# Kernel optimization log

Hardware: AMD Instinct MI355X
Metric: run time of the kernel (lower is better)

## Reference

```python
import jax, jax.numpy as jnp
import numpy as np

IN_DIM, HID, MID, FFN, OUT = 384, 128, 1024, 512, 1024
B, T = 8, 4096
LN_EPS = 1e-5


def _legs_hippo(n: int) -> np.ndarray:
    # A[i, j] = P_i(2j/n - 1) * sqrt(2i + 1), Legendre via 3-term recurrence
    x = 2.0 * np.arange(n) / n - 1.0          # eval points, shape [n]
    P = np.zeros((n, n), dtype=np.float64)     # P[i] = P_i(x)
    P[0] = 1.0
    if n > 1:
        P[1] = x
    for i in range(1, n - 1):
        P[i + 1] = ((2 * i + 1) * x * P[i] - i * P[i - 1]) / (i + 1)
    A = P * np.sqrt(2.0 * np.arange(n) + 1.0)[:, None]
    # rescale so the 4096-step recurrence stays finite (A is a free Parameter,
    # so any test value is valid; unscaled LegS overflows fp32 in ~20 steps)
    s = np.linalg.norm(A, 2)
    return (A / (1.05 * s)).astype(np.float32)


def _layernorm(x, g, b):
    mu = jnp.mean(x, axis=-1, keepdims=True)
    var = jnp.var(x, axis=-1, keepdims=True)
    return (x - mu) * jax.lax.rsqrt(var + LN_EPS) * g + b


def setup_inputs() -> dict:
    key = jax.random.key(0)
    ks = jax.random.split(key, 16)

    def w(k, shape, fan_in):
        return jax.random.normal(k, shape, jnp.float32) * (1.0 / np.sqrt(fan_in))

    return {
        "padded_x": jax.random.normal(ks[0], (B, T, IN_DIM), jnp.float32),
        "seq_lens": jax.random.randint(ks[1], (B,), 1, T + 1, jnp.int32),
        "A": jnp.asarray(_legs_hippo(HID)),
        "enc_w1": w(ks[2], (IN_DIM, MID), IN_DIM), "enc_b1": jnp.zeros((MID,), jnp.float32),
        "enc_w2": w(ks[3], (MID, HID), MID), "enc_b2": jnp.zeros((HID,), jnp.float32),
        "proj_w": w(ks[4], (HID, MID), HID), "proj_b": jnp.zeros((MID,), jnp.float32),
        "ln1_g": jnp.ones((MID,), jnp.float32), "ln1_b": jnp.zeros((MID,), jnp.float32),
        "ffn_w1": w(ks[5], (MID, FFN), MID), "ffn_b1": jnp.zeros((FFN,), jnp.float32),
        "ffn_w2": w(ks[6], (FFN, OUT), FFN), "ffn_b2": jnp.zeros((OUT,), jnp.float32),
        "ln2_g": jnp.ones((OUT,), jnp.float32), "ln2_b": jnp.zeros((OUT,), jnp.float32),
        "out_w": w(ks[7], (OUT, OUT), OUT), "out_b": jnp.zeros((OUT,), jnp.float32),
    }


def reference(padded_x, seq_lens, A, enc_w1, enc_b1, enc_w2, enc_b2,
              proj_w, proj_b, ln1_g, ln1_b, ffn_w1, ffn_b1, ffn_w2, ffn_b2,
              ln2_g, ln2_b, out_w, out_b):
    # encoder: Linear -> GELU(exact) -> Linear   [B, T, HID]
    h_mid = jax.nn.gelu(padded_x @ enc_w1 + enc_b1, approximate=False)
    seqs_bx = h_mid @ enc_w2 + enc_b2

    # masked linear recurrence h_t = A @ h_{t-1} + Bx_t via lax.scan over time
    xs = jnp.swapaxes(seqs_bx, 0, 1)           # [T, B, HID]
    ts = jnp.arange(xs.shape[0])

    def step(h, inp):
        x_t, t = inp
        upd = h @ A.T + x_t                     # (A @ h)^T batched
        mask = (t < seq_lens)[:, None]          # [B, 1]
        return jnp.where(mask, upd, h), None

    h0 = jnp.zeros((padded_x.shape[0], A.shape[0]), padded_x.dtype)
    batch_h, _ = jax.lax.scan(step, h0, (xs, ts))

    # decoder
    projected = batch_h @ proj_w + proj_b
    norm_h = _layernorm(projected, ln1_g, ln1_b)
    ffn_out = jax.nn.gelu(norm_h @ ffn_w1 + ffn_b1, approximate=False) @ ffn_w2 + ffn_b2
    ffn_out = ffn_out + projected               # residual (requires OUT == MID)
    norm_ffn = _layernorm(ffn_out, ln2_g, ln2_b)
    return norm_ffn @ out_w + out_b             # [B, OUT]
```

## Files before the change

kernel.cpp:

```cpp
#include <hip/hip_runtime.h>

typedef __attribute__((ext_vector_type(8))) short short8;
typedef __attribute__((ext_vector_type(4))) short short4v;
typedef __attribute__((ext_vector_type(4))) float float4v;

__device__ __forceinline__ float bf2f(short s) {
  union { float f; unsigned u; } cv; cv.u = ((unsigned)(unsigned short)s) << 16; return cv.f;
}
__device__ __forceinline__ short f2bf(float f) {
  union { float f; unsigned u; } cv; cv.f = f;
  unsigned u = cv.u;
  unsigned r = u + 0x7FFFu + ((u >> 16) & 1u);
  return (short)(r >> 16);
}
__device__ __forceinline__ float gelu_f(float v) {
  return 0.5f * v * (1.0f + erff(v * 0.70710678118654752440f));
}
__device__ __forceinline__ void glds16(const short* g, short* l) {
  __builtin_amdgcn_global_load_lds(
      (const __attribute__((address_space(1))) void*)g,
      (__attribute__((address_space(3))) void*)l, 16, 0, 0);
}

__global__ __launch_bounds__(256) void enc_fused(
    const short* __restrict__ xB, const short* __restrict__ w1T,
    const short* __restrict__ w2T, const float* __restrict__ b1,
    float* __restrict__ encP, const int* __restrict__ seq_lens)
{
  int m0 = blockIdx.x * 64;
  { int b = m0 >> 12, t = m0 & 4095; if (t >= seq_lens[b]) return; }
  int nc0 = blockIdx.y * 2;

  __shared__ __align__(16) short As[64 * 64];
  __shared__ __align__(16) short Ws[128 * 64];
  __shared__ __align__(16) short midb[64 * 128];

  int tid = threadIdx.x, lane = tid & 63, wave = tid >> 6;
  int l15 = lane & 15, quad = lane >> 4;
  int lr = lane >> 3, lseg = lane & 7;

  float4v accO[4][2];
#pragma unroll
  for (int i = 0; i < 4; i++)
#pragma unroll
    for (int j = 0; j < 2; j++) accO[i][j] = 0;

  for (int nci = 0; nci < 2; ++nci) {
    int nc = nc0 + nci;
    float4v accM[4][2];
#pragma unroll
    for (int i = 0; i < 4; i++)
#pragma unroll
      for (int j = 0; j < 2; j++) accM[i][j] = 0;

    for (int ks = 0; ks < 6; ++ks) {
      int kk = ks * 64;
#pragma unroll
      for (int i = 0; i < 2; i++) {
        int rowg = wave * 16 + i * 8;
        glds16(xB + (size_t)(m0 + rowg + lr) * 384 + kk + (lseg ^ lr) * 8, &As[rowg * 64]);
      }
#pragma unroll
      for (int i = 0; i < 4; i++) {
        int rowg = wave * 32 + i * 8;
        glds16(w1T + (size_t)(nc * 128 + rowg + lr) * 384 + kk + (lseg ^ lr) * 8, &Ws[rowg * 64]);
      }
      __syncthreads();
#pragma unroll
      for (int kh = 0; kh < 2; kh++) {
        int s = kh * 4 + quad;
        short8 af[4], bfr[2];
#pragma unroll
        for (int im = 0; im < 4; im++) {
          int r = im * 16 + l15;
          af[im] = *(short8*)&As[r * 64 + ((s ^ (r & 7)) * 8)];
        }
#pragma unroll
        for (int in = 0; in < 2; in++) {
          int r = wave * 32 + in * 16 + l15;
          bfr[in] = *(short8*)&Ws[r * 64 + ((s ^ (r & 7)) * 8)];
        }
#pragma unroll
        for (int im = 0; im < 4; im++)
#pragma unroll
          for (int in = 0; in < 2; in++)
            accM[im][in] = __builtin_amdgcn_mfma_f32_16x16x32_bf16(af[im], bfr[in], accM[im][in], 0, 0, 0);
      }
      __syncthreads();
    }
#pragma unroll
    for (int im = 0; im < 4; im++)
#pragma unroll
      for (int in = 0; in < 2; in++) {
        int k = wave * 32 + in * 16 + l15;
        float bias = b1[nc * 128 + k];
#pragma unroll
        for (int reg = 0; reg < 4; reg++) {
          int m = im * 16 + quad * 4 + reg;
          float v = gelu_f(accM[im][in][reg] + bias);
          int s = k >> 3;
          int sw = (s & 8) | ((s & 7) ^ (m & 7));
          midb[m * 128 + sw * 8 + (k & 7)] = f2bf(v);
        }
      }
    __syncthreads();
#pragma unroll
    for (int ks2 = 0; ks2 < 2; ++ks2) {
      int kk = nc * 128 + ks2 * 64;
#pragma unroll
      for (int i = 0; i < 4; i++) {
        int rowg = wave * 32 + i * 8;
        glds16(w2T + (size_t)(rowg + lr) * 1024 + kk + (lseg ^ lr) * 8, &Ws[rowg * 64]);
      }
      __syncthreads();
#pragma unroll
      for (int kh = 0; kh < 2; kh++) {
        short8 af[4], bfr[2];
#pragma unroll
        for (int im = 0; im < 4; im++) {
          int m = im * 16 + l15;
          int kb = ks2 * 64 + kh * 32 + quad * 8;
          int s = kb >> 3;
          int sw = (s & 8) | ((s & 7) ^ (m & 7));
          af[im] = *(short8*)&midb[m * 128 + sw * 8];
        }
#pragma unroll
        for (int in = 0; in < 2; in++) {
          int r = wave * 32 + in * 16 + l15;
          int s = kh * 4 + quad;
          bfr[in] = *(short8*)&Ws[r * 64 + ((s ^ (r & 7)) * 8)];
        }
#pragma unroll
        for (int im = 0; im < 4; im++)
#pragma unroll
          for (int in = 0; in < 2; in++)
            accO[im][in] = __builtin_amdgcn_mfma_f32_16x16x32_bf16(af[im], bfr[in], accO[im][in], 0, 0, 0);
      }
      __syncthreads();
    }
  }
  float* outp = encP + ((size_t)blockIdx.y << 22);
#pragma unroll
  for (int im = 0; im < 4; im++)
#pragma unroll
    for (int in = 0; in < 2; in++) {
      int n = wave * 32 + in * 16 + l15;
#pragma unroll
      for (int reg = 0; reg < 4; reg++) {
        int m = m0 + im * 16 + quad * 4 + reg;
        outp[(size_t)m * 128 + n] = accO[im][in][reg];
      }
    }
}

__global__ __launch_bounds__(256) void enc_reduce(
    const float* __restrict__ encP, const float* __restrict__ b2,
    short* __restrict__ seqs, const int* __restrict__ seq_lens)
{
  int m0 = blockIdx.x * 64;
  { int b = m0 >> 12, t = m0 & 4095; if (t >= seq_lens[b]) return; }
  int t = threadIdx.x;
#pragma unroll
  for (int i = 0; i < 8; i++) {
    int f4 = t + i * 256;
    int m = m0 + (f4 >> 5);
    int cg = f4 & 31;
    size_t off = (size_t)m * 128 + cg * 4;
    float4v v = *(const float4v*)&encP[off];
#pragma unroll
    for (int y = 1; y < 4; y++) {
      float4v w = *(const float4v*)&encP[((size_t)y << 22) + off];
#pragma unroll
      for (int q = 0; q < 4; q++) v[q] += w[q];
    }
    float4v bb = *(const float4v*)&b2[cg * 4];
    short4v o;
#pragma unroll
    for (int q = 0; q < 4; q++) o[q] = f2bf(v[q] + bb[q]);
    *(short4v*)&seqs[off] = o;
  }
}

__global__ __launch_bounds__(256) void gemm_bt(
    const short* __restrict__ A_, const short* __restrict__ BT,
    float* __restrict__ out, int lda, int ldb, int ldc,
    int kSteps, int kChunk)
{
  int m0 = blockIdx.y * 128;
  int n0 = blockIdx.x * 128;
  int kBase = blockIdx.z * kChunk;

  __shared__ __align__(16) short As[128 * 64];
  __shared__ __align__(16) short Bs[128 * 64];

  int tid = threadIdx.x;
  int lane = tid & 63, wave = tid >> 6;
  int l15 = lane & 15, quad = lane >> 4;
  int wm = wave & 1, wn = wave >> 1;
  int lr = lane >> 3, lseg = lane & 7;

  float4v acc[4][4];
#pragma unroll
  for (int i = 0; i < 4; i++)
#pragma unroll
    for (int j = 0; j < 4; j++) acc[i][j] = 0;

  for (int ks = 0; ks < kSteps; ++ks) {
    int kk = kBase + ks * 64;
#pragma unroll
    for (int i = 0; i < 4; i++) {
      int rowg = wave * 32 + i * 8;
      glds16(A_ + (size_t)(m0 + rowg + lr) * lda + kk + (lseg ^ lr) * 8, &As[rowg * 64]);
      glds16(BT + (size_t)(n0 + rowg + lr) * ldb + kk + (lseg ^ lr) * 8, &Bs[rowg * 64]);
    }
    __syncthreads();
#pragma unroll
    for (int kh = 0; kh < 2; kh++) {
      int s = kh * 4 + quad;
      short8 af[4], bfr[4];
#pragma unroll
      for (int im = 0; im < 4; im++) {
        int r = wm * 64 + im * 16 + l15;
        af[im] = *(short8*)&As[r * 64 + ((s ^ (r & 7)) * 8)];
      }
#pragma unroll
      for (int in = 0; in < 4; in++) {
        int r = wn * 64 + in * 16 + l15;
        bfr[in] = *(short8*)&Bs[r * 64 + ((s ^ (r & 7)) * 8)];
      }
#pragma unroll
      for (int im = 0; im < 4; im++)
#pragma unroll
        for (int in = 0; in < 4; in++)
          acc[im][in] = __builtin_amdgcn_mfma_f32_16x16x32_bf16(af[im], bfr[in], acc[im][in], 0, 0, 0);
    }
    __syncthreads();
  }
  float* outz = out + (size_t)blockIdx.z * 65536;
#pragma unroll
  for (int im = 0; im < 4; im++)
#pragma unroll
    for (int in = 0; in < 4; in++) {
      int n = n0 + wn * 64 + in * 16 + l15;
#pragma unroll
      for (int reg = 0; reg < 4; reg++) {
        int m = m0 + wm * 64 + im * 16 + quad * 4 + reg;
        outz[(size_t)m * ldc + n] = acc[im][in][reg];
      }
    }
}

__global__ void prep_wide(const float* __restrict__ x, const float* __restrict__ w1,
                          const float* __restrict__ w2,
                          const float* __restrict__ proj_w, const float* __restrict__ ffn_w1,
                          const float* __restrict__ ffn_w2, const float* __restrict__ out_w,
                          const float* __restrict__ A, const int* __restrict__ seq_lens,
                          short* __restrict__ xB,
                          short* __restrict__ w1T, short* __restrict__ w2T,
                          short* __restrict__ projB, short* __restrict__ ffn1B,
                          short* __restrict__ ffn2B, short* __restrict__ outB,
                          short* __restrict__ P1, short* __restrict__ P1t,
                          short* __restrict__ P2t,
                          short* __restrict__ Spow, short* __restrict__ SpowT)
{
  int idx = blockIdx.x * 256 + threadIdx.x;
  if (idx < 3145728) {
    int row = idx / 96;
    int t = row & 4095, b = row >> 12;
    if (t >= seq_lens[b]) return;
    float4v v = ((const float4v*)x)[idx];
    short4v o;
#pragma unroll
    for (int j = 0; j < 4; j++) o[j] = f2bf(v[j]);
    ((short4v*)xB)[idx] = o;
    return;
  }
  idx -= 3145728;
  if (idx < 393216) {
    int n = idx / 384, k = idx % 384;
    w1T[idx] = f2bf(w1[k * 1024 + n]);
    return;
  }
  idx -= 393216;
  if (idx < 131072) {
    int n = idx / 1024, k = idx % 1024;
    w2T[idx] = f2bf(w2[k * 128 + n]);
    return;
  }
  idx -= 131072;
  if (idx < 131072) { projB[idx] = f2bf(proj_w[idx]); return; }
  idx -= 131072;
  if (idx < 524288) { ffn1B[idx] = f2bf(ffn_w1[idx]); return; }
  idx -= 524288;
  if (idx < 524288) { ffn2B[idx] = f2bf(ffn_w2[idx]); return; }
  idx -= 524288;
  if (idx < 1048576) { outB[idx] = f2bf(out_w[idx]); return; }
  idx -= 1048576;
  if (idx < 16384) {
    int i = idx >> 7, j = idx & 127;
    short bidv = f2bf((i == j) ? 1.0f : 0.0f);
    P1[i * 8192 + 63 * 128 + j] = bidv;
    P1t[(63 * 128 + j) * 128 + i] = bidv;
    P2t[(63 * 128 + j) * 128 + i] = bidv;
    short ab = f2bf(A[idx]);
    Spow[idx] = ab;
    SpowT[(size_t)j * 128 + i] = ab;
  }
}

__global__ __launch_bounds__(256) void pow_chain(short* __restrict__ Spow,
                                                 short* __restrict__ SpowT)
{
  __shared__ short X[16384];
  __shared__ short XT[16384];
  int t = threadIdx.x;
  for (int i = t * 8; i < 16384; i += 2048) {
    *(short8*)&X[i]  = *(const short8*)&Spow[i];
    *(short8*)&XT[i] = *(const short8*)&SpowT[i];
  }
  __syncthreads();
  int lane = t & 63, wave = t >> 6, l15 = lane & 15, quad = lane >> 4;
  for (int step = 1; step <= 11; ++step) {
    short8 af[2][4], bfr[8][4];
#pragma unroll
    for (int mt = 0; mt < 2; mt++)
#pragma unroll
      for (int ks = 0; ks < 4; ks++)
        af[mt][ks] = *(short8*)&X[(wave * 32 + mt * 16 + l15) * 128 + ks * 32 + quad * 8];
#pragma unroll
    for (int nt = 0; nt < 8; nt++)
#pragma unroll
      for (int ks = 0; ks < 4; ks++)
        bfr[nt][ks] = *(short8*)&XT[(nt * 16 + l15) * 128 + ks * 32 + quad * 8];
    __syncthreads();
    float4v acc[2][8];
#pragma unroll
    for (int mt = 0; mt < 2; mt++)
#pragma unroll
      for (int nt = 0; nt < 8; nt++) acc[mt][nt] = 0;
#pragma unroll
    for (int ks = 0; ks < 4; ks++)
#pragma unroll
      for (int mt = 0; mt < 2; mt++)
#pragma unroll
        for (int nt = 0; nt < 8; nt++)
          acc[mt][nt] = __builtin_amdgcn_mfma_f32_16x16x32_bf16(af[mt][ks], bfr[nt][ks], acc[mt][nt], 0, 0, 0);
    short* gX  = Spow  + (size_t)step * 16384;
    short* gXT = SpowT + (size_t)step * 16384;
#pragma unroll
    for (int mt = 0; mt < 2; mt++)
#pragma unroll
      for (int nt = 0; nt < 8; nt++)
#pragma unroll
        for (int reg = 0; reg < 4; reg++) {
          int m = wave * 32 + mt * 16 + quad * 4 + reg;
          int n = nt * 16 + l15;
          short v = f2bf(acc[mt][nt][reg]);
          X[m * 128 + n] = v; XT[n * 128 + m] = v;
          gX[m * 128 + n] = v; gXT[n * 128 + m] = v;
        }
    __syncthreads();
  }
}

__global__ __launch_bounds__(256) void pow_fill(const short* __restrict__ Spow,
                                                const short* __restrict__ SpowT,
                                                short* __restrict__ P1,
                                                short* __restrict__ P1t,
                                                short* __restrict__ P2t)
{
  __shared__ short cur[16384];
  __shared__ short Bt[16384];
  int bid = blockIdx.x;
  int table1 = bid < 63;
  int e = table1 ? bid + 1 : bid - 62;
  int t = threadIdx.x;
  int lane = t & 63, wave = t >> 6, l15 = lane & 15, quad = lane >> 4;

  int bits = e;
  int k0 = __ffs(bits) - 1; bits &= bits - 1;
  int s0 = table1 ? k0 : (k0 == 0 ? 6 : 6 + k0);
  for (int i = t * 8; i < 16384; i += 2048)
    *(short8*)&cur[i] = *(const short8*)&Spow[(size_t)s0 * 16384 + i];

  while (bits) {
    int k = __ffs(bits) - 1; bits &= bits - 1;
    int si = table1 ? k : (k == 0 ? 6 : 6 + k);
    for (int i = t * 8; i < 16384; i += 2048)
      *(short8*)&Bt[i] = *(const short8*)&SpowT[(size_t)si * 16384 + i];
    __syncthreads();
    short8 af[2][4], bfr[8][4];
#pragma unroll
    for (int mt = 0; mt < 2; mt++)
#pragma unroll
      for (int ks = 0; ks < 4; ks++)
        af[mt][ks] = *(short8*)&cur[(wave * 32 + mt * 16 + l15) * 128 + ks * 32 + quad * 8];
#pragma unroll
    for (int nt = 0; nt < 8; nt++)
#pragma unroll
      for (int ks = 0; ks < 4; ks++)
        bfr[nt][ks] = *(short8*)&Bt[(nt * 16 + l15) * 128 + ks * 32 + quad * 8];
    __syncthreads();
    float4v acc[2][8];
#pragma unroll
    for (int mt = 0; mt < 2; mt++)
#pragma unroll
      for (int nt = 0; nt < 8; nt++) acc[mt][nt] = 0;
#pragma unroll
    for (int ks = 0; ks < 4; ks++)
#pragma unroll
      for (int mt = 0; mt < 2; mt++)
#pragma unroll
        for (int nt = 0; nt < 8; nt++)
          acc[mt][nt] = __builtin_amdgcn_mfma_f32_16x16x32_bf16(af[mt][ks], bfr[nt][ks], acc[mt][nt], 0, 0, 0);
#pragma unroll
    for (int mt = 0; mt < 2; mt++)
#pragma unroll
      for (int nt = 0; nt < 8; nt++)
#pragma unroll
        for (int reg = 0; reg < 4; reg++) {
          int m = wave * 32 + mt * 16 + quad * 4 + reg;
          int n = nt * 16 + l15;
          cur[m * 128 + n] = f2bf(acc[mt][nt][reg]);
        }
    __syncthreads();
  }
  __syncthreads();
  int slot = 63 - e;
  for (int idx = t; idx < 16384; idx += 256) {
    int i = idx >> 7, j = idx & 127;
    short v = cur[idx];
    if (table1) {
      P1[i * 8192 + slot * 128 + j] = v;
      P1t[(slot * 128 + j) * 128 + i] = v;
    } else {
      P2t[(slot * 128 + j) * 128 + i] = v;
    }
  }
}

__global__ __launch_bounds__(256) void combine_gemm(
    const float* __restrict__ Vz, const short* __restrict__ seqs,
    const int* __restrict__ seq_lens,
    const short* __restrict__ P2t, const short* __restrict__ P1t,
    float* __restrict__ hFtail)
{
  __shared__ short X[256 * 8];
  int pp = blockIdx.x >> 5, ks = blockIdx.x & 31;
  int t = threadIdx.x;
  for (int e = t; e < 2048; e += 256) {
    int klocal = e >> 3, b = e & 7;
    int cp = ks * 2 + (klocal >> 7), i = klocal & 127;
    int L = seq_lens[b];
    if (pp == 0) {
      int F = L >> 6, sh = 64 - F;
      float v = 0.f;
      if (cp >= sh) {
        int row = (b * 64 + (cp - sh)) * 128 + i;
#pragma unroll
        for (int z = 0; z < 32; z++) v += Vz[(size_t)z * 65536 + row];
      }
      X[e] = f2bf(v);
    } else {
      int F = L >> 6, rr = L & 63, sh = 64 - rr;
      short s = 0;
      if (cp >= sh) s = seqs[((size_t)b * 4096 + F * 64 + (cp - sh)) * 128 + i];
      X[e] = s;
    }
  }
  __syncthreads();
  const short* P = pp ? P1t : P2t;
  float* outp = hFtail + pp * 1024;
  int i = t & 127, g = t >> 7;
  float acc[4] = {0, 0, 0, 0};
  for (int kl = 0; kl < 256; ++kl) {
    int k = ks * 256 + kl;
    float pv = bf2f(P[k * 128 + i]);
    short4v xv = *(const short4v*)(X + kl * 8 + g * 4);
#pragma unroll
    for (int q = 0; q < 4; q++) acc[q] += bf2f(xv[q]) * pv;
  }
#pragma unroll
  for (int q = 0; q < 4; q++) atomicAdd(&outp[(g * 4 + q) * 128 + i], acc[q]);
}

__global__ __launch_bounds__(256) void proj_stage(
    const float* __restrict__ hFtail, const short* __restrict__ P1t,
    const int* __restrict__ seq_lens, const short* __restrict__ projB,
    const float* __restrict__ proj_b, float* __restrict__ projected)
{
  __shared__ short hT[128 * 8];
  __shared__ float red[4][64][8];
  int t = threadIdx.x;
  {
    int b = t >> 5, i4 = (t & 31) * 4;
    int rr = seq_lens[b] & 63;
    const short* M = P1t + (size_t)(63 - rr) * 128 * 128;
    const float* hF = hFtail + b * 128;
    float acc[4];
#pragma unroll
    for (int q = 0; q < 4; q++) acc[q] = hFtail[1024 + b * 128 + i4 + q];
    for (int j = 0; j < 128; ++j) {
      float hv = hF[j];
      short4v mv = *(const short4v*)&M[j * 128 + i4];
#pragma unroll
      for (int q = 0; q < 4; q++) acc[q] += bf2f(mv[q]) * hv;
    }
#pragma unroll
    for (int q = 0; q < 4; q++) hT[(i4 + q) * 8 + b] = f2bf(acc[q]);
  }
  __syncthreads();
  int c = t & 63, sl = t >> 6;
  int n = blockIdx.x * 64 + c;
  float acc[8] = {0, 0, 0, 0, 0, 0, 0, 0};
  for (int k = sl * 32; k < sl * 32 + 32; ++k) {
    short8 xv = *(short8*)&hT[k * 8];
    float wv = bf2f(projB[k * 1024 + n]);
#pragma unroll
    for (int b = 0; b < 8; b++) acc[b] += bf2f(xv[b]) * wv;
  }
#pragma unroll
  for (int b = 0; b < 8; b++) red[sl][c][b] = acc[b];
  __syncthreads();
  if (sl == 0) {
#pragma unroll
    for (int s = 1; s < 4; s++)
#pragma unroll
      for (int b = 0; b < 8; b++) acc[b] += red[s][c][b];
    float bn = proj_b[n];
#pragma unroll
    for (int b = 0; b < 8; b++) projected[b * 1024 + n] = acc[b] + bn;
  }
}

__global__ __launch_bounds__(256) void ffn1_stage(
    const float* __restrict__ projected, const float* __restrict__ g1,
    const float* __restrict__ b1, const short* __restrict__ ffn1B,
    float* __restrict__ ffn1raw)
{
  __shared__ float part[8][32][2];
  __shared__ float stats[8][2];
  __shared__ short xT[256 * 8];
  __shared__ float red[4][64][8];
  int t = threadIdx.x;
  { int b = t >> 5, j0 = t & 31; float s = 0, q = 0;
    for (int k = j0 * 32; k < j0 * 32 + 32; ++k) { float v = projected[b * 1024 + k]; s += v; q += v * v; }
    part[b][j0][0] = s; part[b][j0][1] = q; }
  __syncthreads();
  if (t < 8) {
    float s = 0, q = 0;
    for (int j = 0; j < 32; j++) { s += part[t][j][0]; q += part[t][j][1]; }
    float mu = s * (1.0f / 1024.0f);
    float var = q * (1.0f / 1024.0f) - mu * mu;
    stats[t][0] = mu; stats[t][1] = rsqrtf(var + 1e-5f);
  }
  __syncthreads();
  int ky0 = blockIdx.y * 256;
  for (int idx = t; idx < 2048; idx += 256) {
    int kl = idx >> 3, b = idx & 7; int k = ky0 + kl;
    float v = (projected[b * 1024 + k] - stats[b][0]) * stats[b][1] * g1[k] + b1[k];
    xT[kl * 8 + b] = f2bf(v);
  }
  __syncthreads();
  int c = t & 63, sl = t >> 6;
  int n = blockIdx.x * 64 + c;
  float acc[8] = {0, 0, 0, 0, 0, 0, 0, 0};
  for (int kl = sl * 64; kl < sl * 64 + 64; ++kl) {
    short8 xv = *(short8*)&xT[kl * 8];
    float wv = bf2f(ffn1B[(size_t)(ky0 + kl) * 512 + n]);
#pragma unroll
    for (int b = 0; b < 8; b++) acc[b] += bf2f(xv[b]) * wv;
  }
#pragma unroll
  for (int b = 0; b < 8; b++) red[sl][c][b] = acc[b];
  __syncthreads();
  if (sl == 0) {
#pragma unroll
    for (int s = 1; s < 4; s++)
#pragma unroll
      for (int b = 0; b < 8; b++) acc[b] += red[s][c][b];
#pragma unroll
    for (int b = 0; b < 8; b++) atomicAdd(&ffn1raw[b * 512 + n], acc[b]);
  }
}

__global__ __launch_bounds__(256) void ffn2_stage(
    const float* __restrict__ ffn1raw, const float* __restrict__ fb1,
    const short* __restrict__ ffn2B, float* __restrict__ ffn2raw)
{
  __shared__ short xT[256 * 8];
  __shared__ float red[4][64][8];
  int t = threadIdx.x;
  int ky0 = blockIdx.y * 256;
  for (int idx = t; idx < 2048; idx += 256) {
    int kl = idx >> 3, b = idx & 7; int k = ky0 + kl;
    float v = gelu_f(ffn1raw[b * 512 + k] + fb1[k]);
    xT[kl * 8 + b] = f2bf(v);
  }
  __syncthreads();
  int c = t & 63, sl = t >> 6;
  int n = blockIdx.x * 64 + c;
  float acc[8] = {0, 0, 0, 0, 0, 0, 0, 0};
  for (int kl = sl * 64; kl < sl * 64 + 64; ++kl) {
    short8 xv = *(short8*)&xT[kl * 8];
    float wv = bf2f(ffn2B[(size_t)(ky0 + kl) * 1024 + n]);
#pragma unroll
    for (int b = 0; b < 8; b++) acc[b] += bf2f(xv[b]) * wv;
  }
#pragma unroll
  for (int b = 0; b < 8; b++) red[sl][c][b] = acc[b];
  __syncthreads();
  if (sl == 0) {
#pragma unroll
    for (int s = 1; s < 4; s++)
#pragma unroll
      for (int b = 0; b < 8; b++) acc[b] += red[s][c][b];
#pragma unroll
    for (int b = 0; b < 8; b++) atomicAdd(&ffn2raw[b * 1024 + n], acc[b]);
  }
}

__global__ __launch_bounds__(256) void out_stage(
    const float* __restrict__ ffn2raw, const float* __restrict__ fb2,
    const float* __restrict__ projected, const float* __restrict__ g2,
    const float* __restrict__ b2ln, const short* __restrict__ outB,
    const float* __restrict__ out_b, float* __restrict__ d_out)
{
  __shared__ float part[8][32][2];
  __shared__ float stats[8][2];
  __shared__ short xT[512 * 8];
  __shared__ float red[4][64][8];
  int t = threadIdx.x;
  { int b = t >> 5, j0 = t & 31; float s = 0, q = 0;
    for (int k = j0 * 32; k < j0 * 32 + 32; ++k) {
      float v = ffn2raw[b * 1024 + k] + fb2[k] + projected[b * 1024 + k];
      s += v; q += v * v;
    }
    part[b][j0][0] = s; part[b][j0][1] = q; }
  __syncthreads();
  if (t < 8) {
    float s = 0, q = 0;
    for (int j = 0; j < 32; j++) { s += part[t][j][0]; q += part[t][j][1]; }
    float mu = s * (1.0f / 1024.0f);
    float var = q * (1.0f / 1024.0f) - mu * mu;
    stats[t][0] = mu; stats[t][1] = rsqrtf(var + 1e-5f);
  }
  __syncthreads();
  int ky0 = blockIdx.y * 512;
  for (int idx = t; idx < 4096; idx += 256) {
    int kl = idx >> 3, b = idx & 7; int k = ky0 + kl;
    float v = ffn2raw[b * 1024 + k] + fb2[k] + projected[b * 1024 + k];
    v = (v - stats[b][0]) * stats[b][1] * g2[k] + b2ln[k];
    xT[kl * 8 + b] = f2bf(v);
  }
  __syncthreads();
  int c = t & 63, sl = t >> 6;
  int n = blockIdx.x * 64 + c;
  float acc[8] = {0, 0, 0, 0, 0, 0, 0, 0};
  for (int kl = sl * 128; kl < sl * 128 + 128; ++kl) {
    short8 xv = *(short8*)&xT[kl * 8];
    float wv = bf2f(outB[(size_t)(ky0 + kl) * 1024 + n]);
#pragma unroll
    for (int b = 0; b < 8; b++) acc[b] += bf2f(xv[b]) * wv;
  }
#pragma unroll
  for (int b = 0; b < 8; b++) red[sl][c][b] = acc[b];
  __syncthreads();
  if (sl == 0) {
#pragma unroll
    for (int s = 1; s < 4; s++)
#pragma unroll
      for (int b = 0; b < 8; b++) acc[b] += red[s][c][b];
    float bn = (blockIdx.y == 0) ? out_b[n] : 0.0f;
#pragma unroll
    for (int b = 0; b < 8; b++) atomicAdd(&d_out[b * 1024 + n], acc[b] + bn);
  }
}

extern "C" void kernel_launch(void* const* d_in, const int* in_sizes, int n_in,
                              void* d_out, int out_size, void* d_ws, size_t ws_size,
                              hipStream_t stream)
{
  (void)in_sizes; (void)n_in; (void)out_size; (void)ws_size;
  const float* x      = (const float*)d_in[0];
  const int* seq_lens = (const int*)d_in[1];
  const float* A      = (const float*)d_in[2];
  const float* enc_w1 = (const float*)d_in[3];
  const float* enc_b1 = (const float*)d_in[4];
  const float* enc_w2 = (const float*)d_in[5];
  const float* enc_b2 = (const float*)d_in[6];
  const float* proj_w = (const float*)d_in[7];
  const float* proj_b = (const float*)d_in[8];
  const float* ln1_g  = (const float*)d_in[9];
  const float* ln1_b  = (const float*)d_in[10];
  const float* ffn_w1 = (const float*)d_in[11];
  const float* ffn_b1 = (const float*)d_in[12];
  const float* ffn_w2 = (const float*)d_in[13];
  const float* ffn_b2 = (const float*)d_in[14];
  const float* ln2_g  = (const float*)d_in[15];
  const float* ln2_b  = (const float*)d_in[16];
  const float* out_w  = (const float*)d_in[17];
  const float* out_b  = (const float*)d_in[18];

  char* p = (char*)d_ws;
  auto alloc = [&](size_t bytes) { char* r = p; p += (bytes + 255) & ~(size_t)255; return r; };
  short* xB    = (short*)alloc(32768ull * 384 * 2);
  float* encP  = (float*)alloc(4ull * 32768 * 128 * 4);
  short* seqs  = (short*)alloc(32768ull * 128 * 2);
  short* w1T   = (short*)alloc(1024ull * 384 * 2);
  short* w2T   = (short*)alloc(128ull * 1024 * 2);
  short* projB = (short*)alloc(128ull * 1024 * 2);
  short* ffn1B = (short*)alloc(1024ull * 512 * 2);
  short* ffn2B = (short*)alloc(512ull * 1024 * 2);
  short* outB  = (short*)alloc(1024ull * 1024 * 2);
  short* Spow  = (short*)alloc(12ull * 16384 * 2);
  short* SpowT = (short*)alloc(12ull * 16384 * 2);
  short* P1    = (short*)alloc(128ull * 8192 * 2);
  short* P1t   = (short*)alloc(8192ull * 128 * 2);
  short* P2t   = (short*)alloc(8192ull * 128 * 2);
  float* Vz    = (float*)alloc(32ull * 512 * 128 * 4);
  float* hFtail  = (float*)alloc(2ull * 8 * 128 * 4);
  float* ffn1raw = (float*)alloc(8ull * 512 * 4);
  float* ffn2raw = (float*)alloc(8ull * 1024 * 4);
  float* projected = (float*)alloc(8ull * 1024 * 4);

  hipMemsetAsync(hFtail, 0, (2ull * 8 * 128 + 8ull * 512 + 8ull * 1024) * 4, stream);
  hipMemsetAsync(d_out, 0, 8192ull * 4, stream);

  prep_wide<<<23104, 256, 0, stream>>>(x, enc_w1, enc_w2, proj_w, ffn_w1, ffn_w2, out_w, A,
      seq_lens, xB, w1T, w2T, projB, ffn1B, ffn2B, outB, P1, P1t, P2t, Spow, SpowT);
  pow_chain<<<1, 256, 0, stream>>>(Spow, SpowT);
  pow_fill<<<126, 256, 0, stream>>>(Spow, SpowT, P1, P1t, P2t);

  enc_fused<<<dim3(512, 4), 256, 0, stream>>>(xB, w1T, w2T, enc_b1, encP, seq_lens);
  enc_reduce<<<512, 256, 0, stream>>>(encP, enc_b2, seqs, seq_lens);

  gemm_bt<<<dim3(1, 4, 32), 256, 0, stream>>>(seqs, P1, Vz, 8192, 8192, 128, 4, 256);
  combine_gemm<<<64, 256, 0, stream>>>(Vz, seqs, seq_lens, P2t, P1t, hFtail);

  proj_stage<<<16, 256, 0, stream>>>(hFtail, P1t, seq_lens, projB, proj_b, projected);
  ffn1_stage<<<dim3(8, 4), 256, 0, stream>>>(projected, ln1_g, ln1_b, ffn1B, ffn1raw);
  ffn2_stage<<<dim3(16, 2), 256, 0, stream>>>(ffn1raw, ffn_b1, ffn2B, ffn2raw);
  out_stage<<<dim3(16, 2), 256, 0, stream>>>(ffn2raw, ffn_b2, projected, ln2_g, ln2_b,
      outB, out_b, (float*)d_out);
}
```

Measured before the change: 405.4 us.

## Fuse post-encoder stages into persistent kernel with grid-wide atomic barriers

Merges the power-chain, power fill, scan GEMMs, projection and decoder stages into one persistent 128-block kernel separated by atomic-counter grid barriers. The encoder reduction is folded into enc_fused through a last-arriving-block counter, and the memsets move into prep_wide. The aim is to remove many kernel launch gaps and tiny-grid tail effects. In exchange it relies on spin-wait barriers that assume all 128 blocks are co-resident, and the power computation is restructured so each block recomputes its powers independently.

```diff
diff --git a/kernel.cpp b/kernel.cpp
--- a/kernel.cpp
+++ b/kernel.cpp
@@ -21,233 +21,8 @@
       (const __attribute__((address_space(1))) void*)g,
       (__attribute__((address_space(3))) void*)l, 16, 0, 0);
 }
-
-__global__ __launch_bounds__(256) void enc_fused(
-    const short* __restrict__ xB, const short* __restrict__ w1T,
-    const short* __restrict__ w2T, const float* __restrict__ b1,
-    float* __restrict__ encP, const int* __restrict__ seq_lens)
-{
-  int m0 = blockIdx.x * 64;
-  { int b = m0 >> 12, t = m0 & 4095; if (t >= seq_lens[b]) return; }
-  int nc0 = blockIdx.y * 2;
-
-  __shared__ __align__(16) short As[64 * 64];
-  __shared__ __align__(16) short Ws[128 * 64];
-  __shared__ __align__(16) short midb[64 * 128];
-
-  int tid = threadIdx.x, lane = tid & 63, wave = tid >> 6;
-  int l15 = lane & 15, quad = lane >> 4;
-  int lr = lane >> 3, lseg = lane & 7;
-
-  float4v accO[4][2];
-#pragma unroll
-  for (int i = 0; i < 4; i++)
-#pragma unroll
-    for (int j = 0; j < 2; j++) accO[i][j] = 0;
-
-  for (int nci = 0; nci < 2; ++nci) {
-    int nc = nc0 + nci;
-    float4v accM[4][2];
-#pragma unroll
-    for (int i = 0; i < 4; i++)
-#pragma unroll
-      for (int j = 0; j < 2; j++) accM[i][j] = 0;
-
-    for (int ks = 0; ks < 6; ++ks) {
-      int kk = ks * 64;
-#pragma unroll
-      for (int i = 0; i < 2; i++) {
-        int rowg = wave * 16 + i * 8;
-        glds16(xB + (size_t)(m0 + rowg + lr) * 384 + kk + (lseg ^ lr) * 8, &As[rowg * 64]);
-      }
-#pragma unroll
-      for (int i = 0; i < 4; i++) {
-        int rowg = wave * 32 + i * 8;
-        glds16(w1T + (size_t)(nc * 128 + rowg + lr) * 384 + kk + (lseg ^ lr) * 8, &Ws[rowg * 64]);
-      }
-      __syncthreads();
-#pragma unroll
-      for (int kh = 0; kh < 2; kh++) {
-        int s = kh * 4 + quad;
-        short8 af[4], bfr[2];
-#pragma unroll
-        for (int im = 0; im < 4; im++) {
-          int r = im * 16 + l15;
-          af[im] = *(short8*)&As[r * 64 + ((s ^ (r & 7)) * 8)];
-        }
-#pragma unroll
-        for (int in = 0; in < 2; in++) {
-          int r = wave * 32 + in * 16 + l15;
-          bfr[in] = *(short8*)&Ws[r * 64 + ((s ^ (r & 7)) * 8)];
-        }
-#pragma unroll
-        for (int im = 0; im < 4; im++)
-#pragma unroll
-          for (int in = 0; in < 2; in++)
-            accM[im][in] = __builtin_amdgcn_mfma_f32_16x16x32_bf16(af[im], bfr[in], accM[im][in], 0, 0, 0);
-      }
-      __syncthreads();
-    }
-#pragma unroll
-    for (int im = 0; im < 4; im++)
-#pragma unroll
-      for (int in = 0; in < 2; in++) {
-        int k = wave * 32 + in * 16 + l15;
-        float bias = b1[nc * 128 + k];
-#pragma unroll
-        for (int reg = 0; reg < 4; reg++) {
-          int m = im * 16 + quad * 4 + reg;
-          float v = gelu_f(accM[im][in][reg] + bias);
-          int s = k >> 3;
-          int sw = (s & 8) | ((s & 7) ^ (m & 7));
-          midb[m * 128 + sw * 8 + (k & 7)] = f2bf(v);
-        }
-      }
-    __syncthreads();
-#pragma unroll
-    for (int ks2 = 0; ks2 < 2; ++ks2) {
-      int kk = nc * 128 + ks2 * 64;
-#pragma unroll
-      for (int i = 0; i < 4; i++) {
-        int rowg = wave * 32 + i * 8;
-        glds16(w2T + (size_t)(rowg + lr) * 1024 + kk + (lseg ^ lr) * 8, &Ws[rowg * 64]);
-      }
-      __syncthreads();
-#pragma unroll
-      for (int kh = 0; kh < 2; kh++) {
-        short8 af[4], bfr[2];
-#pragma unroll
-        for (int im = 0; im < 4; im++) {
-          int m = im * 16 + l15;
-          int kb = ks2 * 64 + kh * 32 + quad * 8;
-          int s = kb >> 3;
-          int sw = (s & 8) | ((s & 7) ^ (m & 7));
-          af[im] = *(short8*)&midb[m * 128 + sw * 8];
-        }
-#pragma unroll
-        for (int in = 0; in < 2; in++) {
-          int r = wave * 32 + in * 16 + l15;
-          int s = kh * 4 + quad;
-          bfr[in] = *(short8*)&Ws[r * 64 + ((s ^ (r & 7)) * 8)];
-        }
-#pragma unroll
-        for (int im = 0; im < 4; im++)
-#pragma unroll
-          for (int in = 0; in < 2; in++)
-            accO[im][in] = __builtin_amdgcn_mfma_f32_16x16x32_bf16(af[im], bfr[in], accO[im][in], 0, 0, 0);
-      }
-      __syncthreads();
-    }
-  }
-  float* outp = encP + ((size_t)blockIdx.y << 22);
-#pragma unroll
-  for (int im = 0; im < 4; im++)
-#pragma unroll
-    for (int in = 0; in < 2; in++) {
-      int n = wave * 32 + in * 16 + l15;
-#pragma unroll
-      for (int reg = 0; reg < 4; reg++) {
-        int m = m0 + im * 16 + quad * 4 + reg;
-        outp[(size_t)m * 128 + n] = accO[im][in][reg];
-      }
-    }
-}
-
-__global__ __launch_bounds__(256) void enc_reduce(
-    const float* __restrict__ encP, const float* __restrict__ b2,
-    short* __restrict__ seqs, const int* __restrict__ seq_lens)
-{
-  int m0 = blockIdx.x * 64;
-  { int b = m0 >> 12, t = m0 & 4095; if (t >= seq_lens[b]) return; }
-  int t = threadIdx.x;
-#pragma unroll
-  for (int i = 0; i < 8; i++) {
-    int f4 = t + i * 256;
-    int m = m0 + (f4 >> 5);
-    int cg = f4 & 31;
-    size_t off = (size_t)m * 128 + cg * 4;
-    float4v v = *(const float4v*)&encP[off];
-#pragma unroll
-    for (int y = 1; y < 4; y++) {
-      float4v w = *(const float4v*)&encP[((size_t)y << 22) + off];
-#pragma unroll
-      for (int q = 0; q < 4; q++) v[q] += w[q];
-    }
-    float4v bb = *(const float4v*)&b2[cg * 4];
-    short4v o;
-#pragma unroll
-    for (int q = 0; q < 4; q++) o[q] = f2bf(v[q] + bb[q]);
-    *(short4v*)&seqs[off] = o;
-  }
-}
-
-__global__ __launch_bounds__(256) void gemm_bt(
-    const short* __restrict__ A_, const short* __restrict__ BT,
-    float* __restrict__ out, int lda, int ldb, int ldc,
-    int kSteps, int kChunk)
-{
-  int m0 = blockIdx.y * 128;
-  int n0 = blockIdx.x * 128;
-  int kBase = blockIdx.z * kChunk;
-
-  __shared__ __align__(16) short As[128 * 64];
-  __shared__ __align__(16) short Bs[128 * 64];
-
-  int tid = threadIdx.x;
-  int lane = tid & 63, wave = tid >> 6;
-  int l15 = lane & 15, quad = lane >> 4;
-  int wm = wave & 1, wn = wave >> 1;
-  int lr = lane >> 3, lseg = lane & 7;
-
-  float4v acc[4][4];
-#pragma unroll
-  for (int i = 0; i < 4; i++)
-#pragma unroll
-    for (int j = 0; j < 4; j++) acc[i][j] = 0;
-
-  for (int ks = 0; ks < kSteps; ++ks) {
-    int kk = kBase + ks * 64;
-#pragma unroll
-    for (int i = 0; i < 4; i++) {
-      int rowg = wave * 32 + i * 8;
-      glds16(A_ + (size_t)(m0 + rowg + lr) * lda + kk + (lseg ^ lr) * 8, &As[rowg * 64]);
-      glds16(BT + (size_t)(n0 + rowg + lr) * ldb + kk + (lseg ^ lr) * 8, &Bs[rowg * 64]);
-    }
-    __syncthreads();
-#pragma unroll
-    for (int kh = 0; kh < 2; kh++) {
-      int s = kh * 4 + quad;
-      short8 af[4], bfr[4];
-#pragma unroll
-      for (int im = 0; im < 4; im++) {
-        int r = wm * 64 + im * 16 + l15;
-        af[im] = *(short8*)&As[r * 64 + ((s ^ (r & 7)) * 8)];
-      }
-#pragma unroll
-      for (int in = 0; in < 4; in++) {
-        int r = wn * 64 + in * 16 + l15;
-        bfr[in] = *(short8*)&Bs[r * 64 + ((s ^ (r & 7)) * 8)];
-      }
-#pragma unroll
-      for (int im = 0; im < 4; im++)
-#pragma unroll
-        for (int in = 0; in < 4; in++)
-          acc[im][in] = __builtin_amdgcn_mfma_f32_16x16x32_bf16(af[im], bfr[in], acc[im][in], 0, 0, 0);
-    }
-    __syncthreads();
-  }
-  float* outz = out + (size_t)blockIdx.z * 65536;
-#pragma unroll
-  for (int im = 0; im < 4; im++)
-#pragma unroll
-    for (int in = 0; in < 4; in++) {
-      int n = n0 + wn * 64 + in * 16 + l15;
-#pragma unroll
-      for (int reg = 0; reg < 4; reg++) {
-        int m = m0 + wm * 64 + im * 16 + quad * 4 + reg;
-        outz[(size_t)m * ldc + n] = acc[im][in][reg];
-      }
-    }
+__device__ __forceinline__ int swz(int r, int c) {
+  return r * 128 + ((((c >> 3) ^ (r & 7)) << 3) | (c & 7));
 }
 
 __global__ void prep_wide(const float* __restrict__ x, const float* __restrict__ w1,
@@ -261,7 +36,8 @@
                           short* __restrict__ ffn2B, short* __restrict__ outB,
                           short* __restrict__ P1, short* __restrict__ P1t,
                           short* __restrict__ P2t,
-                          short* __restrict__ Spow, short* __restrict__ SpowT)
+                          float* __restrict__ hFtail, int* __restrict__ encCnt,
+                          int* __restrict__ gcnt)
 {
   int idx = blockIdx.x * 256 + threadIdx.x;
   if (idx < 3145728) {
@@ -298,382 +74,561 @@
   idx -= 1048576;
   if (idx < 16384) {
     int i = idx >> 7, j = idx & 127;
-    short bidv = f2bf((i == j) ? 1.0f : 0.0f);
-    P1[i * 8192 + 63 * 128 + j] = bidv;
-    P1t[(63 * 128 + j) * 128 + i] = bidv;
-    P2t[(63 * 128 + j) * 128 + i] = bidv;
+    short idv = f2bf((i == j) ? 1.0f : 0.0f);
+    P1[i * 8192 + 63 * 128 + j] = idv;
+    P1t[(63 * 128 + j) * 128 + i] = idv;
+    P2t[(63 * 128 + j) * 128 + i] = idv;
     short ab = f2bf(A[idx]);
-    Spow[idx] = ab;
-    SpowT[(size_t)j * 128 + i] = ab;
-  }
-}
-
-__global__ __launch_bounds__(256) void pow_chain(short* __restrict__ Spow,
-                                                 short* __restrict__ SpowT)
+    P1[i * 8192 + 62 * 128 + j] = ab;
+    P1t[(62 * 128 + j) * 128 + i] = ab;
+    return;
+  }
+  idx -= 16384;
+  if (idx < 2048) { hFtail[idx] = 0.f; return; }
+  idx -= 2048;
+  if (idx < 512) { encCnt[idx] = 0; return; }
+  idx -= 512;
+  if (idx < 16) gcnt[idx] = 0;
+}
+
+__global__ __launch_bounds__(256) void enc_fused(
+    const short* __restrict__ xB, const short* __restrict__ w1T,
+    const short* __restrict__ w2T, const float* __restrict__ b1,
+    const float* __restrict__ b2, float* __restrict__ encP,
+    short* __restrict__ seqs, int* __restrict__ encCnt,
+    const int* __restrict__ seq_lens)
 {
-  __shared__ short X[16384];
-  __shared__ short XT[16384];
-  int t = threadIdx.x;
-  for (int i = t * 8; i < 16384; i += 2048) {
-    *(short8*)&X[i]  = *(const short8*)&Spow[i];
-    *(short8*)&XT[i] = *(const short8*)&SpowT[i];
-  }
+  int m0 = blockIdx.x * 64;
+  { int b = m0 >> 12, t = m0 & 4095; if (t >= seq_lens[b]) return; }
+  int nc0 = blockIdx.y * 2;
+
+  __shared__ __align__(16) short As[64 * 64];
+  __shared__ __align__(16) short Ws[128 * 64];
+  __shared__ __align__(16) short midb[64 * 128];
+  __shared__ int lastf;
+
+  int tid = threadIdx.x, lane = tid & 63, wave = tid >> 6;
+  int l15 = lane & 15, quad = lane >> 4;
+  int lr = lane >> 3, lseg = lane & 7;
+
+  float4v accO[4][2];
+#pragma unroll
+  for (int i = 0; i < 4; i++)
+#pragma unroll
+    for (int j = 0; j < 2; j++) accO[i][j] = 0;
+
+  for (int nci = 0; nci < 2; ++nci) {
+    int nc = nc0 + nci;
+    float4v accM[4][2];
+#pragma unroll
+    for (int i = 0; i < 4; i++)
+#pragma unroll
+      for (int j = 0; j < 2; j++) accM[i][j] = 0;
+
+    for (int ks = 0; ks < 6; ++ks) {
+      int kk = ks * 64;
+#pragma unroll
+      for (int i = 0; i < 2; i++) {
+        int rowg = wave * 16 + i * 8;
+        glds16(xB + (size_t)(m0 + rowg + lr) * 384 + kk + (lseg ^ lr) * 8, &As[rowg * 64]);
+      }
+#pragma unroll
+      for (int i = 0; i < 4; i++) {
+        int rowg = wave * 32 + i * 8;
+        glds16(w1T + (size_t)(nc * 128 + rowg + lr) * 384 + kk + (lseg ^ lr) * 8, &Ws[rowg * 64]);
+      }
+      __syncthreads();
+#pragma unroll
+      for (int kh = 0; kh < 2; kh++) {
+        int s = kh * 4 + quad;
+        short8 af[4], bfr[2];
+#pragma unroll
+        for (int im = 0; im < 4; im++) {
+          int r = im * 16 + l15;
+          af[im] = *(short8*)&As[r * 64 + ((s ^ (r & 7)) * 8)];
+        }
+#pragma unroll
+        for (int in = 0; in < 2; in++) {
+          int r = wave * 32 + in * 16 + l15;
+          bfr[in] = *(short8*)&Ws[r * 64 + ((s ^ (r & 7)) * 8)];
+        }
+#pragma unroll
+        for (int im = 0; im < 4; im++)
+#pragma unroll
+          for (int in = 0; in < 2; in++)
+            accM[im][in] = __builtin_amdgcn_mfma_f32_16x16x32_bf16(af[im], bfr[in], accM[im][in], 0, 0, 0);
+      }
+      __syncthreads();
+    }
+#pragma unroll
+    for (int im = 0; im < 4; im++)
+#pragma unroll
+      for (int in = 0; in < 2; in++) {
+        int k = wave * 32 + in * 16 + l15;
+        float bias = b1[nc * 128 + k];
+#pragma unroll
+        for (int reg = 0; reg < 4; reg++) {
+          int m = im * 16 + quad * 4 + reg;
+          float v = gelu_f(accM[im][in][reg] + bias);
+          int s = k >> 3;
+          int sw = (s & 8) | ((s & 7) ^ (m & 7));
+          midb[m * 128 + sw * 8 + (k & 7)] = f2bf(v);
+        }
+      }
+    __syncthreads();
+#pragma unroll
+    for (int ks2 = 0; ks2 < 2; ++ks2) {
+      int kk = nc * 128 + ks2 * 64;
+#pragma unroll
+      for (int i = 0; i < 4; i++) {
+        int rowg = wave * 32 + i * 8;
+        glds16(w2T + (size_t)(rowg + lr) * 1024 + kk + (lseg ^ lr) * 8, &Ws[rowg * 64]);
+      }
+      __syncthreads();
+#pragma unroll
+      for (int kh = 0; kh < 2; kh++) {
+        short8 af[4], bfr[2];
+#pragma unroll
+        for (int im = 0; im < 4; im++) {
+          int m = im * 16 + l15;
+          int kb = ks2 * 64 + kh * 32 + quad * 8;
+          int s = kb >> 3;
+          int sw = (s & 8) | ((s & 7) ^ (m & 7));
+          af[im] = *(short8*)&midb[m * 128 + sw * 8];
+        }
+#pragma unroll
+        for (int in = 0; in < 2; in++) {
+          int r = wave * 32 + in * 16 + l15;
+          int s = kh * 4 + quad;
+          bfr[in] = *(short8*)&Ws[r * 64 + ((s ^ (r & 7)) * 8)];
+        }
+#pragma unroll
+        for (int im = 0; im < 4; im++)
+#pragma unroll
+          for (int in = 0; in < 2; in++)
+            accO[im][in] = __builtin_amdgcn_mfma_f32_16x16x32_bf16(af[im], bfr[in], accO[im][in], 0, 0, 0);
+      }
+      __syncthreads();
+    }
+  }
+  float* outp = encP + ((size_t)blockIdx.y << 22);
+#pragma unroll
+  for (int im = 0; im < 4; im++)
+#pragma unroll
+    for (int in = 0; in < 2; in++) {
+      int n = wave * 32 + in * 16 + l15;
+#pragma unroll
+      for (int reg = 0; reg < 4; reg++) {
+        int m = m0 + im * 16 + quad * 4 + reg;
+        outp[(size_t)m * 128 + n] = accO[im][in][reg];
+      }
+    }
+  __threadfence();
+  if (tid == 0) lastf = (atomicAdd(&encCnt[blockIdx.x], 1) == 3);
   __syncthreads();
+  if (lastf) {
+    __threadfence();
+#pragma unroll
+    for (int i = 0; i < 8; i++) {
+      int f4 = tid + i * 256;
+      int m = m0 + (f4 >> 5);
+      int cg = f4 & 31;
+      size_t off = (size_t)m * 128 + cg * 4;
+      float4v v = *(const float4v*)&encP[off];
+#pragma unroll
+      for (int y = 1; y < 4; y++) {
+        float4v w = *(const float4v*)&encP[((size_t)y << 22) + off];
+#pragma unroll
+        for (int q = 0; q < 4; q++) v[q] += w[q];
+      }
+      float4v bb = *(const float4v*)&b2[cg * 4];
+      short4v o;
+#pragma unroll
+      for (int q = 0; q < 4; q++) o[q] = f2bf(v[q] + bb[q]);
+      *(short4v*)&seqs[off] = o;
+    }
+  }
+}
+
+__device__ __forceinline__ void gsync(int* c, int n) {
+  __threadfence();
+  __syncthreads();
+  if (threadIdx.x == 0) {
+    atomicAdd(c, 1);
+    while (atomicAdd(c, 0) < n) __builtin_amdgcn_s_sleep(8);
+  }
+  __syncthreads();
+  __threadfence();
+}
+
+__global__ __launch_bounds__(256) void mega(
+    const float* __restrict__ A, const int* __restrict__ seq_lens,
+    short* __restrict__ P1, short* __restrict__ P1t, short* __restrict__ P2t,
+    const short* __restrict__ seqs, float* __restrict__ Vz, float* __restrict__ hFtail,
+    const short* __restrict__ projB, const float* __restrict__ proj_b,
+    float* __restrict__ projected,
+    const float* __restrict__ g1, const float* __restrict__ b1ln,
+    const short* __restrict__ ffn1B, float* __restrict__ ffn1raw,
+    const float* __restrict__ fb1, const short* __restrict__ ffn2B,
+    float* __restrict__ ffn2raw, const float* __restrict__ fb2,
+    const float* __restrict__ g2, const float* __restrict__ b2ln,
+    const short* __restrict__ outB, const float* __restrict__ out_b,
+    float* __restrict__ d_out, int* __restrict__ gcnt)
+{
+  __shared__ __align__(16) char smem[65536];
+  int bid = blockIdx.x, t = threadIdx.x;
   int lane = t & 63, wave = t >> 6, l15 = lane & 15, quad = lane >> 4;
-  for (int step = 1; step <= 11; ++step) {
-    short8 af[2][4], bfr[8][4];
-#pragma unroll
-    for (int mt = 0; mt < 2; mt++)
+
+  if (bid < 126) {
+    short* cur  = (short*)smem;
+    short* curT = cur + 16384;
+    const short* ATg = P1t + (size_t)62 * 16384;
+    for (int i = t; i < 16384; i += 256) {
+      int r = i >> 7, c = i & 127;
+      short v = f2bf(A[i]);
+      cur[swz(r, c)] = v;
+      curT[swz(c, r)] = v;
+    }
+    __syncthreads();
+    int table1 = bid < 63;
+    int e = table1 ? bid + 1 : bid - 62;
+    int E = table1 ? e : (e << 6);
+    int mk = 31 - __clz(E);
+    auto mmstep = [&](const short* YT, bool gB) {
+      short8 af[2][4], bfv[8][4];
+#pragma unroll
+      for (int mt = 0; mt < 2; mt++)
+#pragma unroll
+        for (int ks = 0; ks < 4; ks++) {
+          int r = wave * 32 + mt * 16 + l15, s = ks * 4 + quad;
+          af[mt][ks] = *(const short8*)&cur[r * 128 + ((s ^ (r & 7)) << 3)];
+        }
+#pragma unroll
+      for (int nt = 0; nt < 8; nt++)
+#pragma unroll
+        for (int ks = 0; ks < 4; ks++) {
+          int n = nt * 16 + l15;
+          if (gB) bfv[nt][ks] = *(const short8*)&YT[n * 128 + ks * 32 + quad * 8];
+          else {
+            int s = ks * 4 + quad;
+            bfv[nt][ks] = *(const short8*)&YT[n * 128 + ((s ^ (n & 7)) << 3)];
+          }
+        }
+      __syncthreads();
+      float4v acc[2][8];
+#pragma unroll
+      for (int mt = 0; mt < 2; mt++)
+#pragma unroll
+        for (int nt = 0; nt < 8; nt++) acc[mt][nt] = 0;
 #pragma unroll
       for (int ks = 0; ks < 4; ks++)
-        af[mt][ks] = *(short8*)&X[(wave * 32 + mt * 16 + l15) * 128 + ks * 32 + quad * 8];
-#pragma unroll
-    for (int nt = 0; nt < 8; nt++)
-#pragma unroll
-      for (int ks = 0; ks < 4; ks++)
-        bfr[nt][ks] = *(short8*)&XT[(nt * 16 + l15) * 128 + ks * 32 + quad * 8];
-    __syncthreads();
-    float4v acc[2][8];
-#pragma unroll
-    for (int mt = 0; mt < 2; mt++)
-#pragma unroll
-      for (int nt = 0; nt < 8; nt++) acc[mt][nt] = 0;
-#pragma unroll
-    for (int ks = 0; ks < 4; ks++)
+#pragma unroll
+        for (int mt = 0; mt < 2; mt++)
+#pragma unroll
+          for (int nt = 0; nt < 8; nt++)
+            acc[mt][nt] = __builtin_amdgcn_mfma_f32_16x16x32_bf16(af[mt][ks], bfv[nt][ks], acc[mt][nt], 0, 0, 0);
 #pragma unroll
       for (int mt = 0; mt < 2; mt++)
 #pragma unroll
         for (int nt = 0; nt < 8; nt++)
-          acc[mt][nt] = __builtin_amdgcn_mfma_f32_16x16x32_bf16(af[mt][ks], bfr[nt][ks], acc[mt][nt], 0, 0, 0);
-    short* gX  = Spow  + (size_t)step * 16384;
-    short* gXT = SpowT + (size_t)step * 16384;
-#pragma unroll
-    for (int mt = 0; mt < 2; mt++)
-#pragma unroll
-      for (int nt = 0; nt < 8; nt++)
+#pragma unroll
+          for (int reg = 0; reg < 4; reg++) {
+            int m = wave * 32 + mt * 16 + quad * 4 + reg;
+            int n = nt * 16 + l15;
+            short v = f2bf(acc[mt][nt][reg]);
+            cur[swz(m, n)] = v;
+            curT[swz(n, m)] = v;
+          }
+      __syncthreads();
+    };
+    for (int k = mk - 1; k >= 0; --k) {
+      mmstep(curT, false);
+      if ((E >> k) & 1) mmstep(ATg, true);
+    }
+    int slot = 63 - e;
+    if (!(table1 && e == 1)) {
+      for (int i = t; i < 16384; i += 256) {
+        int r = i >> 7, c = i & 127;
+        short v = cur[swz(r, c)];
+        if (table1) {
+          P1[r * 8192 + slot * 128 + c] = v;
+          P1t[(slot * 128 + c) * 128 + r] = v;
+        } else {
+          P2t[(slot * 128 + c) * 128 + r] = v;
+        }
+      }
+    }
+  }
+  gsync(&gcnt[0], 128);
+
+  {
+    short* As = (short*)smem;
+    short* Bs = As + 8192;
+    int z = bid & 31, mt0 = bid >> 5;
+    int m0 = mt0 * 128, kBase = z * 256;
+    int wm = wave & 1, wn = wave >> 1, lr = lane >> 3, lseg = lane & 7;
+    float4v acc[4][4];
+#pragma unroll
+    for (int i = 0; i < 4; i++)
+#pragma unroll
+      for (int j = 0; j < 4; j++) acc[i][j] = 0;
+    for (int ks = 0; ks < 4; ++ks) {
+      int kk = kBase + ks * 64;
+#pragma unroll
+      for (int i = 0; i < 4; i++) {
+        int rowg = wave * 32 + i * 8;
+        glds16(seqs + (size_t)(m0 + rowg + lr) * 8192 + kk + (lseg ^ lr) * 8, &As[rowg * 64]);
+        glds16(P1 + (size_t)(rowg + lr) * 8192 + kk + (lseg ^ lr) * 8, &Bs[rowg * 64]);
+      }
+      __syncthreads();
+#pragma unroll
+      for (int kh = 0; kh < 2; kh++) {
+        int s = kh * 4 + quad;
+        short8 af[4], bfr[4];
+#pragma unroll
+        for (int im = 0; im < 4; im++) {
+          int r = wm * 64 + im * 16 + l15;
+          af[im] = *(short8*)&As[r * 64 + ((s ^ (r & 7)) * 8)];
+        }
+#pragma unroll
+        for (int in = 0; in < 4; in++) {
+          int r = wn * 64 + in * 16 + l15;
+          bfr[in] = *(short8*)&Bs[r * 64 + ((s ^ (r & 7)) * 8)];
+        }
+#pragma unroll
+        for (int im = 0; im < 4; im++)
+#pragma unroll
+          for (int in = 0; in < 4; in++)
+            acc[im][in] = __builtin_amdgcn_mfma_f32_16x16x32_bf16(af[im], bfr[in], acc[im][in], 0, 0, 0);
+      }
+      __syncthreads();
+    }
+    float* outz = Vz + (size_t)z * 65536;
+#pragma unroll
+    for (int im = 0; im < 4; im++)
+#pragma unroll
+      for (int in = 0; in < 4; in++) {
+        int n = wn * 64 + in * 16 + l15;
 #pragma unroll
         for (int reg = 0; reg < 4; reg++) {
-          int m = wave * 32 + mt * 16 + quad * 4 + reg;
-          int n = nt * 16 + l15;
-          short v = f2bf(acc[mt][nt][reg]);
-          X[m * 128 + n] = v; XT[n * 128 + m] = v;
-          gX[m * 128 + n] = v; gXT[n * 128 + m] = v;
-        }
-    __syncthreads();
-  }
-}
-
-__global__ __launch_bounds__(256) void pow_fill(const short* __restrict__ Spow,
-                                                const short* __restrict__ SpowT,
-                                                short* __restrict__ P1,
-                                                short* __restrict__ P1t,
-                                                short* __restrict__ P2t)
-{
-  __shared__ short cur[16384];
-  __shared__ short Bt[16384];
-  int bid = blockIdx.x;
-  int table1 = bid < 63;
-  int e = table1 ? bid + 1 : bid - 62;
-  int t = threadIdx.x;
-  int lane = t & 63, wave = t >> 6, l15 = lane & 15, quad = lane >> 4;
-
-  int bits = e;
-  int k0 = __ffs(bits) - 1; bits &= bits - 1;
-  int s0 = table1 ? k0 : (k0 == 0 ? 6 : 6 + k0);
-  for (int i = t * 8; i < 16384; i += 2048)
-    *(short8*)&cur[i] = *(const short8*)&Spow[(size_t)s0 * 16384 + i];
-
-  while (bits) {
-    int k = __ffs(bits) - 1; bits &= bits - 1;
-    int si = table1 ? k : (k == 0 ? 6 : 6 + k);
-    for (int i = t * 8; i < 16384; i += 2048)
-      *(short8*)&Bt[i] = *(const short8*)&SpowT[(size_t)si * 16384 + i];
-    __syncthreads();
-    short8 af[2][4], bfr[8][4];
-#pragma unroll
-    for (int mt = 0; mt < 2; mt++)
-#pragma unroll
-      for (int ks = 0; ks < 4; ks++)
-        af[mt][ks] = *(short8*)&cur[(wave * 32 + mt * 16 + l15) * 128 + ks * 32 + quad * 8];
-#pragma unroll
-    for (int nt = 0; nt < 8; nt++)
-#pragma unroll
-      for (int ks = 0; ks < 4; ks++)
-        bfr[nt][ks] = *(short8*)&Bt[(nt * 16 + l15) * 128 + ks * 32 + quad * 8];
-    __syncthreads();
-    float4v acc[2][8];
-#pragma unroll
-    for (int mt = 0; mt < 2; mt++)
-#pragma unroll
-      for (int nt = 0; nt < 8; nt++) acc[mt][nt] = 0;
-#pragma unroll
-    for (int ks = 0; ks < 4; ks++)
-#pragma unroll
-      for (int mt = 0; mt < 2; mt++)
-#pragma unroll
-        for (int nt = 0; nt < 8; nt++)
-          acc[mt][nt] = __builtin_amdgcn_mfma_f32_16x16x32_bf16(af[mt][ks], bfr[nt][ks], acc[mt][nt], 0, 0, 0);
-#pragma unroll
-    for (int mt = 0; mt < 2; mt++)
-#pragma unroll
-      for (int nt = 0; nt < 8; nt++)
-#pragma unroll
-        for (int reg = 0; reg < 4; reg++) {
-          int m = wave * 32 + mt * 16 + quad * 4 + reg;
-          int n = nt * 16 + l15;
-          cur[m * 128 + n] = f2bf(acc[mt][nt][reg]);
-        }
-    __syncthreads();
-  }
-  __syncthreads();
-  int slot = 63 - e;
-  for (int idx = t; idx < 16384; idx += 256) {
-    int i = idx >> 7, j = idx & 127;
-    short v = cur[idx];
-    if (table1) {
-      P1[i * 8192 + slot * 128 + j] = v;
-      P1t[(slot * 128 + j) * 128 + i] = v;
-    } else {
-      P2t[(slot * 128 + j) * 128 + i] = v;
-    }
-  }
-}
-
-__global__ __launch_bounds__(256) void combine_gemm(
-    const float* __restrict__ Vz, const short* __restrict__ seqs,
-    const int* __restrict__ seq_lens,
-    const short* __restrict__ P2t, const short* __restrict__ P1t,
-    float* __restrict__ hFtail)
-{
-  __shared__ short X[256 * 8];
-  int pp = blockIdx.x >> 5, ks = blockIdx.x & 31;
-  int t = threadIdx.x;
-  for (int e = t; e < 2048; e += 256) {
-    int klocal = e >> 3, b = e & 7;
-    int cp = ks * 2 + (klocal >> 7), i = klocal & 127;
-    int L = seq_lens[b];
-    if (pp == 0) {
-      int F = L >> 6, sh = 64 - F;
-      float v = 0.f;
-      if (cp >= sh) {
-        int row = (b * 64 + (cp - sh)) * 128 + i;
-#pragma unroll
-        for (int z = 0; z < 32; z++) v += Vz[(size_t)z * 65536 + row];
-      }
-      X[e] = f2bf(v);
-    } else {
-      int F = L >> 6, rr = L & 63, sh = 64 - rr;
-      short s = 0;
-      if (cp >= sh) s = seqs[((size_t)b * 4096 + F * 64 + (cp - sh)) * 128 + i];
-      X[e] = s;
-    }
-  }
-  __syncthreads();
-  const short* P = pp ? P1t : P2t;
-  float* outp = hFtail + pp * 1024;
-  int i = t & 127, g = t >> 7;
-  float acc[4] = {0, 0, 0, 0};
-  for (int kl = 0; kl < 256; ++kl) {
-    int k = ks * 256 + kl;
-    float pv = bf2f(P[k * 128 + i]);
-    short4v xv = *(const short4v*)(X + kl * 8 + g * 4);
-#pragma unroll
-    for (int q = 0; q < 4; q++) acc[q] += bf2f(xv[q]) * pv;
-  }
-#pragma unroll
-  for (int q = 0; q < 4; q++) atomicAdd(&outp[(g * 4 + q) * 128 + i], acc[q]);
-}
-
-__global__ __launch_bounds__(256) void proj_stage(
-    const float* __restrict__ hFtail, const short* __restrict__ P1t,
-    const int* __restrict__ seq_lens, const short* __restrict__ projB,
-    const float* __restrict__ proj_b, float* __restrict__ projected)
-{
-  __shared__ short hT[128 * 8];
-  __shared__ float red[4][64][8];
-  int t = threadIdx.x;
-  {
-    int b = t >> 5, i4 = (t & 31) * 4;
-    int rr = seq_lens[b] & 63;
-    const short* M = P1t + (size_t)(63 - rr) * 128 * 128;
-    const float* hF = hFtail + b * 128;
-    float acc[4];
-#pragma unroll
-    for (int q = 0; q < 4; q++) acc[q] = hFtail[1024 + b * 128 + i4 + q];
-    for (int j = 0; j < 128; ++j) {
-      float hv = hF[j];
-      short4v mv = *(const short4v*)&M[j * 128 + i4];
-#pragma unroll
-      for (int q = 0; q < 4; q++) acc[q] += bf2f(mv[q]) * hv;
-    }
-#pragma unroll
-    for (int q = 0; q < 4; q++) hT[(i4 + q) * 8 + b] = f2bf(acc[q]);
-  }
-  __syncthreads();
-  int c = t & 63, sl = t >> 6;
-  int n = blockIdx.x * 64 + c;
-  float acc[8] = {0, 0, 0, 0, 0, 0, 0, 0};
-  for (int k = sl * 32; k < sl * 32 + 32; ++k) {
-    short8 xv = *(short8*)&hT[k * 8];
-    float wv = bf2f(projB[k * 1024 + n]);
-#pragma unroll
-    for (int b = 0; b < 8; b++) acc[b] += bf2f(xv[b]) * wv;
-  }
-#pragma unroll
-  for (int b = 0; b < 8; b++) red[sl][c][b] = acc[b];
-  __syncthreads();
-  if (sl == 0) {
-#pragma unroll
-    for (int s = 1; s < 4; s++)
-#pragma unroll
-      for (int b = 0; b < 8; b++) acc[b] += red[s][c][b];
-    float bn = proj_b[n];
-#pragma unroll
-    for (int b = 0; b < 8; b++) projected[b * 1024 + n] = acc[b] + bn;
-  }
-}
-
-__global__ __launch_bounds__(256) void ffn1_stage(
-    const float* __restrict__ projected, const float* __restrict__ g1,
-    const float* __restrict__ b1, const short* __restrict__ ffn1B,
-    float* __restrict__ ffn1raw)
-{
-  __shared__ float part[8][32][2];
-  __shared__ float stats[8][2];
-  __shared__ short xT[256 * 8];
-  __shared__ float red[4][64][8];
-  int t = threadIdx.x;
-  { int b = t >> 5, j0 = t & 31; float s = 0, q = 0;
-    for (int k = j0 * 32; k < j0 * 32 + 32; ++k) { float v = projected[b * 1024 + k]; s += v; q += v * v; }
-    part[b][j0][0] = s; part[b][j0][1] = q; }
-  __syncthreads();
-  if (t < 8) {
-    float s = 0, q = 0;
-    for (int j = 0; j < 32; j++) { s += part[t][j][0]; q += part[t][j][1]; }
-    float mu = s * (1.0f / 1024.0f);
-    float var = q * (1.0f / 1024.0f) - mu * mu;
-    stats[t][0] = mu; stats[t][1] = rsqrtf(var + 1e-5f);
-  }
-  __syncthreads();
-  int ky0 = blockIdx.y * 256;
-  for (int idx = t; idx < 2048; idx += 256) {
-    int kl = idx >> 3, b = idx & 7; int k = ky0 + kl;
-    float v = (projected[b * 1024 + k] - stats[b][0]) * stats[b][1] * g1[k] + b1[k];
-    xT[kl * 8 + b] = f2bf(v);
-  }
-  __syncthreads();
-  int c = t & 63, sl = t >> 6;
-  int n = blockIdx.x * 64 + c;
-  float acc[8] = {0, 0, 0, 0, 0, 0, 0, 0};
-  for (int kl = sl * 64; kl < sl * 64 + 64; ++kl) {
-    short8 xv = *(short8*)&xT[kl * 8];
-    float wv = bf2f(ffn1B[(size_t)(ky0 + kl) * 512 + n]);
-#pragma unroll
-    for (int b = 0; b < 8; b++) acc[b] += bf2f(xv[b]) * wv;
-  }
-#pragma unroll
-  for (int b = 0; b < 8; b++) red[sl][c][b] = acc[b];
-  __syncthreads();
-  if (sl == 0) {
-#pragma unroll
-    for (int s = 1; s < 4; s++)
-#pragma unroll
-      for (int b = 0; b < 8; b++) acc[b] += red[s][c][b];
-#pragma unroll
-    for (int b = 0; b < 8; b++) atomicAdd(&ffn1raw[b * 512 + n], acc[b]);
-  }
-}
-
-__global__ __launch_bounds__(256) void ffn2_stage(
-    const float* __restrict__ ffn1raw, const float* __restrict__ fb1,
-    const short* __restrict__ ffn2B, float* __restrict__ ffn2raw)
-{
-  __shared__ short xT[256 * 8];
-  __shared__ float red[4][64][8];
-  int t = threadIdx.x;
-  int ky0 = blockIdx.y * 256;
-  for (int idx = t; idx < 2048; idx += 256) {
-    int kl = idx >> 3, b = idx & 7; int k = ky0 + kl;
-    float v = gelu_f(ffn1raw[b * 512 + k] + fb1[k]);
-    xT[kl * 8 + b] = f2bf(v);
-  }
-  __syncthreads();
-  int c = t & 63, sl = t >> 6;
-  int n = blockIdx.x * 64 + c;
-  float acc[8] = {0, 0, 0, 0, 0, 0, 0, 0};
-  for (int kl = sl * 64; kl < sl * 64 + 64; ++kl) {
-    short8 xv = *(short8*)&xT[kl * 8];
-    float wv = bf2f(ffn2B[(size_t)(ky0 + kl) * 1024 + n]);
-#pragma unroll
-    for (int b = 0; b < 8; b++) acc[b] += bf2f(xv[b]) * wv;
-  }
-#pragma unroll
-  for (int b = 0; b < 8; b++) red[sl][c][b] = acc[b];
-  __syncthreads();
-  if (sl == 0) {
-#pragma unroll
-    for (int s = 1; s < 4; s++)
-#pragma unroll
-      for (int b = 0; b < 8; b++) acc[b] += red[s][c][b];
-#pragma unroll
-    for (int b = 0; b < 8; b++) atomicAdd(&ffn2raw[b * 1024 + n], acc[b]);
-  }
-}
-
-__global__ __launch_bounds__(256) void out_stage(
-    const float* __restrict__ ffn2raw, const float* __restrict__ fb2,
-    const float* __restrict__ projected, const float* __restrict__ g2,
-    const float* __restrict__ b2ln, const short* __restrict__ outB,
-    const float* __restrict__ out_b, float* __restrict__ d_out)
-{
-  __shared__ float part[8][32][2];
-  __shared__ float stats[8][2];
-  __shared__ short xT[512 * 8];
-  __shared__ float red[4][64][8];
-  int t = threadIdx.x;
-  { int b = t >> 5, j0 = t & 31; float s = 0, q = 0;
-    for (int k = j0 * 32; k < j0 * 32 + 32; ++k) {
+          int m = m0 + wm * 64 + im * 16 + quad * 4 + reg;
+          outz[(size_t)m * 128 + n] = acc[im][in][reg];
+        }
+      }
+  }
+  gsync(&gcnt[1], 128);
+
+  if (bid < 64) {
+    short* X = (short*)smem;
+    int pp = bid >> 5, ks = bid & 31;
+    for (int e = t; e < 2048; e += 256) {
+      int klocal = e >> 3, b = e & 7;
+      int cp = ks * 2 + (klocal >> 7), i = klocal & 127;
+      int L = seq_lens[b];
+      if (pp == 0) {
+        int F = L >> 6, sh = 64 - F;
+        float v = 0.f;
+        if (cp >= sh) {
+          int row = (b * 64 + (cp - sh)) * 128 + i;
+#pragma unroll
+          for (int z = 0; z < 32; z++) v += Vz[(size_t)z * 65536 + row];
+        }
+        X[e] = f2bf(v);
+      } else {
+        int F = L >> 6, rr = L & 63, sh = 64 - rr;
+        short s = 0;
+        if (cp >= sh) s = seqs[((size_t)b * 4096 + F * 64 + (cp - sh)) * 128 + i];
+        X[e] = s;
+      }
+    }
+    __syncthreads();
+    const short* P = pp ? P1t : P2t;
+    float* outp = hFtail + pp * 1024;
+    int i = t & 127, g = t >> 7;
+    float acc[4] = {0, 0, 0, 0};
+    for (int kl = 0; kl < 256; ++kl) {
+      int k = ks * 256 + kl;
+      float pv = bf2f(P[k * 128 + i]);
+      short4v xv = *(const short4v*)(X + kl * 8 + g * 4);
+#pragma unroll
+      for (int q = 0; q < 4; q++) acc[q] += bf2f(xv[q]) * pv;
+    }
+#pragma unroll
+    for (int q = 0; q < 4; q++) atomicAdd(&outp[(g * 4 + q) * 128 + i], acc[q]);
+  }
+  gsync(&gcnt[2], 128);
+
+  if (bid < 16) {
+    short* hT = (short*)smem;
+    float (*red)[64][8] = (float(*)[64][8])(smem + 4096);
+    {
+      int b = t >> 5, i4 = (t & 31) * 4;
+      int rr = seq_lens[b] & 63;
+      const short* M = P1t + (size_t)(63 - rr) * 16384;
+      const float* hF = hFtail + b * 128;
+      float acc[4];
+#pragma unroll
+      for (int q = 0; q < 4; q++) acc[q] = hFtail[1024 + b * 128 + i4 + q];
+      for (int j = 0; j < 128; ++j) {
+        float hv = hF[j];
+        short4v mv = *(const short4v*)&M[j * 128 + i4];
+#pragma unroll
+        for (int q = 0; q < 4; q++) acc[q] += bf2f(mv[q]) * hv;
+      }
+#pragma unroll
+      for (int q = 0; q < 4; q++) hT[(i4 + q) * 8 + b] = f2bf(acc[q]);
+    }
+    __syncthreads();
+    int c = t & 63, sl = t >> 6;
+    int n = bid * 64 + c;
+    float acc[8] = {0, 0, 0, 0, 0, 0, 0, 0};
+    for (int k = sl * 32; k < sl * 32 + 32; ++k) {
+      short8 xv = *(short8*)&hT[k * 8];
+      float wv = bf2f(projB[k * 1024 + n]);
+#pragma unroll
+      for (int b = 0; b < 8; b++) acc[b] += bf2f(xv[b]) * wv;
+    }
+#pragma unroll
+    for (int b = 0; b < 8; b++) red[sl][c][b] = acc[b];
+    __syncthreads();
+    if (sl == 0) {
+#pragma unroll
+      for (int s = 1; s < 4; s++)
+#pragma unroll
+        for (int b = 0; b < 8; b++) acc[b] += red[s][c][b];
+      float bn = proj_b[n];
+#pragma unroll
+      for (int b = 0; b < 8; b++) projected[b * 1024 + n] = acc[b] + bn;
+    }
+  }
+  gsync(&gcnt[3], 128);
+
+  if (bid < 8) {
+    float (*part)[32][2] = (float(*)[32][2])smem;
+    float (*stats)[2] = (float(*)[2])(smem + 2048);
+    short* xT = (short*)(smem + 4096);
+    float (*red)[64][8] = (float(*)[64][8])(smem + 4096 + 16384);
+    { int b = t >> 5, j0 = t & 31; float s = 0, q = 0;
+      for (int k = j0 * 32; k < j0 * 32 + 32; ++k) { float v = projected[b * 1024 + k]; s += v; q += v * v; }
+      part[b][j0][0] = s; part[b][j0][1] = q; }
+    __syncthreads();
+    if (t < 8) {
+      float s = 0, q = 0;
+      for (int j = 0; j < 32; j++) { s += part[t][j][0]; q += part[t][j][1]; }
+      float mu = s * (1.0f / 1024.0f);
+      float var = q * (1.0f / 1024.0f) - mu * mu;
+      stats[t][0] = mu; stats[t][1] = rsqrtf(var + 1e-5f);
+    }
+    __syncthreads();
+    for (int idx = t; idx < 8192; idx += 256) {
+      int k = idx >> 3, b = idx & 7;
+      float v = (projected[b * 1024 + k] - stats[b][0]) * stats[b][1] * g1[k] + b1ln[k];
+      xT[k * 8 + b] = f2bf(v);
+    }
+    __syncthreads();
+    int c = t & 63, sl = t >> 6;
+    int n = bid * 64 + c;
+    float acc[8] = {0, 0, 0, 0, 0, 0, 0, 0};
+    for (int k = sl * 256; k < sl * 256 + 256; ++k) {
+      short8 xv = *(short8*)&xT[k * 8];
+      float wv = bf2f(ffn1B[(size_t)k * 512 + n]);
+#pragma unroll
+      for (int b = 0; b < 8; b++) acc[b] += bf2f(xv[b]) * wv;
+    }
+#pragma unroll
+    for (int b = 0; b < 8; b++) red[sl][c][b] = acc[b];
+    __syncthreads();
+    if (sl == 0) {
+#pragma unroll
+      for (int s = 1; s < 4; s++)
+#pragma unroll
+        for (int b = 0; b < 8; b++) acc[b] += red[s][c][b];
+#pragma unroll
+      for (int b = 0; b < 8; b++) ffn1raw[b * 512 + n] = acc[b];
+    }
+  }
+  gsync(&gcnt[4], 128);
+
+  if (bid < 16) {
+    short* xT = (short*)smem;
+    float (*red)[64][8] = (float(*)[64][8])(smem + 8192);
+    for (int idx = t; idx < 4096; idx += 256) {
+      int k = idx >> 3, b = idx & 7;
+      float v = gelu_f(ffn1raw[b * 512 + k] + fb1[k]);
+      xT[k * 8 + b] = f2bf(v);
+    }
+    __syncthreads();
+    int c = t & 63, sl = t >> 6;
+    int n = bid * 64 + c;
+    float acc[8] = {0, 0, 0, 0, 0, 0, 0, 0};
+    for (int k = sl * 128; k < sl * 128 + 128; ++k) {
+      short8 xv = *(short8*)&xT[k * 8];
+      float wv = bf2f(ffn2B[(size_t)k * 1024 + n]);
+#pragma unroll
+      for (int b = 0; b < 8; b++) acc[b] += bf2f(xv[b]) * wv;
+    }
+#pragma unroll
+    for (int b = 0; b < 8; b++) red[sl][c][b] = acc[b];
+    __syncthreads();
+    if (sl == 0) {
+#pragma unroll
+      for (int s = 1; s < 4; s++)
+#pragma unroll
+        for (int b = 0; b < 8; b++) acc[b] += red[s][c][b];
+#pragma unroll
+      for (int b = 0; b < 8; b++) ffn2raw[b * 1024 + n] = acc[b];
+    }
+  }
+  gsync(&gcnt[5], 128);
+
+  if (bid < 16) {
+    float (*part)[32][2] = (float(*)[32][2])smem;
+    float (*stats)[2] = (float(*)[2])(smem + 2048);
+    short* xT = (short*)(smem + 4096);
+    float (*red)[64][8] = (float(*)[64][8])(smem + 4096 + 16384);
+    { int b = t >> 5, j0 = t & 31; float s = 0, q = 0;
+      for (int k = j0 * 32; k < j0 * 32 + 32; ++k) {
+        float v = ffn2raw[b * 1024 + k] + fb2[k] + projected[b * 1024 + k];
+        s += v; q += v * v;
+      }
+      part[b][j0][0] = s; part[b][j0][1] = q; }
+    __syncthreads();
+    if (t < 8) {
+      float s = 0, q = 0;
+      for (int j = 0; j < 32; j++) { s += part[t][j][0]; q += part[t][j][1]; }
+      float mu = s * (1.0f / 1024.0f);
+      float var = q * (1.0f / 1024.0f) - mu * mu;
+      stats[t][0] = mu; stats[t][1] = rsqrtf(var + 1e-5f);
+    }
+    __syncthreads();
+    for (int idx = t; idx < 8192; idx += 256) {
+      int k = idx >> 3, b = idx & 7;
       float v = ffn2raw[b * 1024 + k] + fb2[k] + projected[b * 1024 + k];
-      s += v; q += v * v;
-    }
-    part[b][j0][0] = s; part[b][j0][1] = q; }
-  __syncthreads();
-  if (t < 8) {
-    float s = 0, q = 0;
-    for (int j = 0; j < 32; j++) { s += part[t][j][0]; q += part[t][j][1]; }
-    float mu = s * (1.0f / 1024.0f);
-    float var = q * (1.0f / 1024.0f) - mu * mu;
-    stats[t][0] = mu; stats[t][1] = rsqrtf(var + 1e-5f);
-  }
-  __syncthreads();
-  int ky0 = blockIdx.y * 512;
-  for (int idx = t; idx < 4096; idx += 256) {
-    int kl = idx >> 3, b = idx & 7; int k = ky0 + kl;
-    float v = ffn2raw[b * 1024 + k] + fb2[k] + projected[b * 1024 + k];
-    v = (v - stats[b][0]) * stats[b][1] * g2[k] + b2ln[k];
-    xT[kl * 8 + b] = f2bf(v);
-  }
-  __syncthreads();
-  int c = t & 63, sl = t >> 6;
-  int n = blockIdx.x * 64 + c;
-  float acc[8] = {0, 0, 0, 0, 0, 0, 0, 0};
-  for (int kl = sl * 128; kl < sl * 128 + 128; ++kl) {
-    short8 xv = *(short8*)&xT[kl * 8];
-    float wv = bf2f(outB[(size_t)(ky0 + kl) * 1024 + n]);
-#pragma unroll
-    for (int b = 0; b < 8; b++) acc[b] += bf2f(xv[b]) * wv;
-  }
-#pragma unroll
-  for (int b = 0; b < 8; b++) red[sl][c][b] = acc[b];
-  __syncthreads();
-  if (sl == 0) {
-#pragma unroll
-    for (int s = 1; s < 4; s++)
-#pragma unroll
-      for (int b = 0; b < 8; b++) acc[b] += red[s][c][b];
-    float bn = (blockIdx.y == 0) ? out_b[n] : 0.0f;
-#pragma unroll
-    for (int b = 0; b < 8; b++) atomicAdd(&d_out[b * 1024 + n], acc[b] + bn);
+      v = (v - stats[b][0]) * stats[b][1] * g2[k] + b2ln[k];
+      xT[k * 8 + b] = f2bf(v);
+    }
+    __syncthreads();
+    int c = t & 63, sl = t >> 6;
+    int n = bid * 64 + c;
+    float acc[8] = {0, 0, 0, 0, 0, 0, 0, 0};
+    for (int k = sl * 256; k < sl * 256 + 256; ++k) {
+      short8 xv = *(short8*)&xT[k * 8];
+      float wv = bf2f(outB[(size_t)k * 1024 + n]);
+#pragma unroll
+      for (int b = 0; b < 8; b++) acc[b] += bf2f(xv[b]) * wv;
+    }
+#pragma unroll
+    for (int b = 0; b < 8; b++) red[sl][c][b] = acc[b];
+    __syncthreads();
+    if (sl == 0) {
+#pragma unroll
+      for (int s = 1; s < 4; s++)
+#pragma unroll
+        for (int b = 0; b < 8; b++) acc[b] += red[s][c][b];
+      float bn = out_b[n];
+#pragma unroll
+      for (int b = 0; b < 8; b++) d_out[b * 1024 + n] = acc[b] + bn;
+    }
   }
 }
 
@@ -713,34 +668,25 @@
   short* ffn1B = (short*)alloc(1024ull * 512 * 2);
   short* ffn2B = (short*)alloc(512ull * 1024 * 2);
   short* outB  = (short*)alloc(1024ull * 1024 * 2);
-  short* Spow  = (short*)alloc(12ull * 16384 * 2);
-  short* SpowT = (short*)alloc(12ull * 16384 * 2);
   short* P1    = (short*)alloc(128ull * 8192 * 2);
   short* P1t   = (short*)alloc(8192ull * 128 * 2);
   short* P2t   = (short*)alloc(8192ull * 128 * 2);
   float* Vz    = (float*)alloc(32ull * 512 * 128 * 4);
-  float* hFtail  = (float*)alloc(2ull * 8 * 128 * 4);
+  float* hFtail  = (float*)alloc(2048ull * 4);
+  float* projected = (float*)alloc(8ull * 1024 * 4);
   float* ffn1raw = (float*)alloc(8ull * 512 * 4);
   float* ffn2raw = (float*)alloc(8ull * 1024 * 4);
-  float* projected = (float*)alloc(8ull * 1024 * 4);
-
-  hipMemsetAsync(hFtail, 0, (2ull * 8 * 128 + 8ull * 512 + 8ull * 1024) * 4, stream);
-  hipMemsetAsync(d_out, 0, 8192ull * 4, stream);
-
-  prep_wide<<<23104, 256, 0, stream>>>(x, enc_w1, enc_w2, proj_w, ffn_w1, ffn_w2, out_w, A,
-      seq_lens, xB, w1T, w2T, projB, ffn1B, ffn2B, outB, P1, P1t, P2t, Spow, SpowT);
-  pow_chain<<<1, 256, 0, stream>>>(Spow, SpowT);
-  pow_fill<<<126, 256, 0, stream>>>(Spow, SpowT, P1, P1t, P2t);
-
-  enc_fused<<<dim3(512, 4), 256, 0, stream>>>(xB, w1T, w2T, enc_b1, encP, seq_lens);
-  enc_reduce<<<512, 256, 0, stream>>>(encP, enc_b2, seqs, seq_lens);
-
-  gemm_bt<<<dim3(1, 4, 32), 256, 0, stream>>>(seqs, P1, Vz, 8192, 8192, 128, 4, 256);
-  combine_gemm<<<64, 256, 0, stream>>>(Vz, seqs, seq_lens, P2t, P1t, hFtail);
-
-  proj_stage<<<16, 256, 0, stream>>>(hFtail, P1t, seq_lens, projB, proj_b, projected);
-  ffn1_stage<<<dim3(8, 4), 256, 0, stream>>>(projected, ln1_g, ln1_b, ffn1B, ffn1raw);
-  ffn2_stage<<<dim3(16, 2), 256, 0, stream>>>(ffn1raw, ffn_b1, ffn2B, ffn2raw);
-  out_stage<<<dim3(16, 2), 256, 0, stream>>>(ffn2raw, ffn_b2, projected, ln2_g, ln2_b,
-      outB, out_b, (float*)d_out);
-}
+  int*   encCnt  = (int*)alloc(512ull * 4);
+  int*   gcnt    = (int*)alloc(16ull * 4);
+
+  prep_wide<<<23115, 256, 0, stream>>>(x, enc_w1, enc_w2, proj_w, ffn_w1, ffn_w2, out_w,
+      A, seq_lens, xB, w1T, w2T, projB, ffn1B, ffn2B, outB, P1, P1t, P2t,
+      hFtail, encCnt, gcnt);
+
+  enc_fused<<<dim3(512, 4), 256, 0, stream>>>(xB, w1T, w2T, enc_b1, enc_b2,
+      encP, seqs, encCnt, seq_lens);
+
+  mega<<<128, 256, 0, stream>>>(A, seq_lens, P1, P1t, P2t, seqs, Vz, hFtail,
+      projB, proj_b, projected, ln1_g, ln1_b, ffn1B, ffn1raw, ffn_b1,
+      ffn2B, ffn2raw, ffn_b2, ln2_g, ln2_b, outB, out_b, (float*)d_out, gcnt);
+}
```

Result: slower. 625.5 us (+54.3%).
